# Kernel tuning notes

Measured on AMD Instinct MI355X. Metric: run time of the kernel, lower is better.

The kernel has to match this reference:

```python
import jax, jax.numpy as jnp
import numpy as np

# --- constants derived from init_kwargs (mirrors Categorical2DSemanticMapModule.__init__) ---
H, W = 480, 640
HFOV = 79
DU = 4                      # du_scale
NSEM = 16                   # num_sem_categories
VR = 100                    # vision_range
XY_RES = Z_RES = 5          # map_resolution (cm per bin)
MIN_DEPTH, MAX_DEPTH = 20.0, 500.0   # cm (0.2m/5.0m * 100)
AGENT_H = 88.0              # camera_height * 100 cm
MIN_VOX = int(-40 / Z_RES)  # -8
MAX_VOX = int(360 / Z_RES)  # 72
ZBINS = MAX_VOX - MIN_VOX   # 80
MIN_MAPPED = int(25 / Z_RES - MIN_VOX)             # 13 (min_obs_height_cm)
MAX_MAPPED = int((AGENT_H + 1) / Z_RES - MIN_VOX)  # 25
MAP_T, EXP_T, CAT_T = 1.0, 1.0, 5.0                # map/exp/cat pred thresholds
DILATE_ITER, DILATE_SIZE = 1, 3
F_PIX = (W / 2.0) / float(np.tan(np.deg2rad(HFOV / 2.0)))
CX, CY = W / 2.0, H / 2.0
B, T = 4, 4
LM = 240   # local map size
GM = 960   # global map size
NMAP = 4 + NSEM  # NON_SEM_CHANNELS + num_sem_categories


def setup_inputs() -> dict:
    key = jax.random.key(0)
    k1, k2 = jax.random.split(key)
    seq_obs = jax.random.uniform(k1, (B, T, 4 + NSEM, H, W), dtype=jnp.float32)
    seq_obs = seq_obs.at[:, :, 3].multiply(600.0)  # depth channel in cm, spans [0, 600)
    seq_pose_delta = jax.random.normal(k2, (B, T, 3), dtype=jnp.float32) * 0.1
    seq_camera_poses = jnp.tile(jnp.eye(4, dtype=jnp.float32)[None], (B, 1, 1))
    return {
        'seq_obs': seq_obs,
        'seq_pose_delta': seq_pose_delta,
        'seq_dones': jnp.zeros((B, T), jnp.int32),
        'seq_update_global': jnp.ones((B, T), jnp.int32),
        'seq_camera_poses': seq_camera_poses,
        'init_local_map': jnp.zeros((B, NMAP, LM, LM), jnp.float32),
        'init_global_map': jnp.zeros((B, NMAP, GM, GM), jnp.float32),
        'init_local_pose': jnp.zeros((B, 3), jnp.float32),
        'init_global_pose': jnp.zeros((B, 3), jnp.float32),
        'init_lmb': jnp.zeros((B, 4), jnp.int32),
        'init_origins': jnp.zeros((B, 3), jnp.float32),
    }


def _ego_map(obs_bt):
    """Core semantic-mapping kernel for one frame.
    obs_bt: (4+NSEM, H, W) -> ego map (2+NSEM, VR, VR).
    depth -> point cloud -> voxel scatter-add -> height projection -> threshold -> dilation.
    """
    depth = obs_bt[3, ::DU, ::DU]        # (h, w) cm
    sem = obs_bt[4:, ::DU, ::DU]         # (NSEM, h, w)
    h, w = depth.shape
    uu, vv = jnp.meshgrid(jnp.arange(w, dtype=jnp.float32) * DU,
                          jnp.arange(h, dtype=jnp.float32) * DU)
    # pinhole back-projection (cm), camera at agent height, elevation 0
    X = (uu - CX) * depth / F_PIX            # lateral
    Zh = AGENT_H + (CY - vv) * depth / F_PIX  # height above floor
    Yf = depth                                # forward range
    valid = (depth > MIN_DEPTH) & (depth < MAX_DEPTH)
    # voxel binning (shift_loc centers agent laterally at VR/2)
    xb = jnp.round(X / XY_RES + VR / 2.0).astype(jnp.int32)
    yb = jnp.round(Yf / XY_RES).astype(jnp.int32)
    zb = jnp.round(Zh / Z_RES).astype(jnp.int32) - MIN_VOX
    valid = valid & (xb >= 0) & (xb < VR) & (yb >= 0) & (yb < VR) & (zb >= 0) & (zb < ZBINS)
    lin = (yb * VR + xb) * ZBINS + zb
    lin = jnp.where(valid, lin, VR * VR * ZBINS)  # route invalid points to a dump bin
    C = 1 + NSEM
    feat = jnp.concatenate([jnp.ones((1, h, w), depth.dtype), sem], 0)  # (C, h, w)
    feat = jnp.where(valid[None], feat, 0.0).reshape(C, -1).T           # (N, C)
    grid = jnp.zeros((VR * VR * ZBINS + 1, C), feat.dtype).at[lin.reshape(-1)].add(feat)
    vox = grid[:-1].reshape(VR, VR, ZBINS, C)
    agent_h = vox[:, :, MIN_MAPPED:MAX_MAPPED].sum(2)  # (VR, VR, C)
    all_h = vox.sum(2)
    obstacle = jnp.clip(agent_h[..., 0] / MAP_T, 0.0, 1.0)
    explored = jnp.clip(all_h[..., 0] / EXP_T, 0.0, 1.0)
    semmap = jnp.clip(all_h[..., 1:] / CAT_T, 0.0, 1.0)
    # morphological dilation of obstacle map (3x3 max, dilate_iter times)
    for _ in range(DILATE_ITER):
        obstacle = jax.lax.reduce_window(obstacle, 0.0, jax.lax.max,
                                         (DILATE_SIZE, DILATE_SIZE), (1, 1), 'SAME')
    return jnp.concatenate([obstacle[None], explored[None], jnp.moveaxis(semmap, -1, 0)], 0)


def reference(seq_obs, seq_pose_delta, seq_dones, seq_update_global, seq_camera_poses,
              init_local_map, init_global_map, init_local_pose, init_global_pose,
              init_lmb, init_origins):
    Bb, Tt = seq_obs.shape[:2]
    flat = seq_obs.reshape((Bb * Tt,) + seq_obs.shape[2:])
    ego = jax.vmap(_ego_map)(flat)                      # (B*T, 2+NSEM, VR, VR)
    return ego.reshape(Bb, Tt, 2 + NSEM, VR, VR)
```

## Files before the change

kernel.cpp:

```cpp
#include <hip/hip_runtime.h>
#include <math.h>

#define IMG_H 480
#define IMG_W 640
#define DU    4
#define SUB_H 120
#define SUB_W 160
#define NSEM  16
#define NCH_IN 20
#define VR    100
#define ZBINS 80
#define MIN_MAPPED 13
#define MAX_MAPPED 25
#define NOUT  18
#define NCELL (VR * VR)

__global__ void scatter_kernel(const float* __restrict__ obs,
                               float* __restrict__ out,
                               float* __restrict__ agent,
                               int nframes, float f_pix) {
    const int npix = SUB_H * SUB_W;
    int tid = blockIdx.x * blockDim.x + threadIdx.x;
    if (tid >= nframes * npix) return;
    int f = tid / npix;
    int p = tid - f * npix;
    int v = p / SUB_W;
    int u = p - v * SUB_W;

    const float* frame = obs + (size_t)f * NCH_IN * IMG_H * IMG_W;
    size_t pix_off = (size_t)(v * DU) * IMG_W + (size_t)(u * DU);

    float depth = frame[(size_t)3 * IMG_H * IMG_W + pix_off];
    if (!(depth > 20.0f && depth < 500.0f)) return;

    float uu = (float)(u * DU);
    float vv = (float)(v * DU);
    float X  = (uu - 320.0f) * depth / f_pix;
    float Zh = 88.0f + (240.0f - vv) * depth / f_pix;

    int xb = (int)rintf(X / 5.0f + 50.0f);
    int yb = (int)rintf(depth / 5.0f);
    int zb = (int)rintf(Zh / 5.0f) + 8;

    if (xb < 0 || xb >= VR || yb < 0 || yb >= VR || zb < 0 || zb >= ZBINS) return;

    int cell = yb * VR + xb;
    float* outf = out + (size_t)f * NOUT * NCELL;

    atomicAdd(&outf[1 * NCELL + cell], 1.0f);
    if (zb >= MIN_MAPPED && zb < MAX_MAPPED)
        atomicAdd(&agent[(size_t)f * NCELL + cell], 1.0f);

    #pragma unroll
    for (int c = 0; c < NSEM; ++c) {
        float s = frame[(size_t)(4 + c) * IMG_H * IMG_W + pix_off];
        atomicAdd(&outf[(2 + c) * NCELL + cell], s);
    }
}

__global__ void finalize_kernel(float* __restrict__ out,
                                const float* __restrict__ agent,
                                int nframes) {
    int tid = blockIdx.x * blockDim.x + threadIdx.x;
    if (tid >= nframes * NCELL) return;
    int f = tid / NCELL;
    int p = tid - f * NCELL;
    int y = p / VR;
    int x = p - y * VR;

    const float* ag = agent + (size_t)f * NCELL;
    float m = 0.0f;
    #pragma unroll
    for (int dy = -1; dy <= 1; ++dy) {
        int yy = y + dy;
        if (yy < 0 || yy >= VR) continue;
        #pragma unroll
        for (int dx = -1; dx <= 1; ++dx) {
            int xx = x + dx;
            if (xx < 0 || xx >= VR) continue;
            m = fmaxf(m, ag[yy * VR + xx]);
        }
    }

    float* outf = out + (size_t)f * NOUT * NCELL;
    outf[p] = fminf(m, 1.0f);

    float e = outf[1 * NCELL + p];
    outf[1 * NCELL + p] = fminf(fmaxf(e, 0.0f), 1.0f);

    #pragma unroll
    for (int c = 0; c < NSEM; ++c) {
        float s = outf[(2 + c) * NCELL + p];
        outf[(2 + c) * NCELL + p] = fminf(fmaxf(s / 5.0f, 0.0f), 1.0f);
    }
}

extern "C" void kernel_launch(void* const* d_in, const int* in_sizes, int n_in,
                              void* d_out, int out_size, void* d_ws, size_t ws_size,
                              hipStream_t stream) {
    const float* obs = (const float*)d_in[0];
    float* out = (float*)d_out;
    float* agent = (float*)d_ws;

    int nframes = in_sizes[0] / (NCH_IN * IMG_H * IMG_W);

    float f_pix = (float)(IMG_W / 2.0 / tan((79.0 / 2.0) * M_PI / 180.0));

    hipMemsetAsync(d_out, 0, (size_t)nframes * NOUT * NCELL * sizeof(float), stream);
    hipMemsetAsync(d_ws, 0, (size_t)nframes * NCELL * sizeof(float), stream);

    int npix_total = nframes * SUB_H * SUB_W;
    scatter_kernel<<<(npix_total + 255) / 256, 256, 0, stream>>>(
        obs, out, agent, nframes, f_pix);

    int ncell_total = nframes * NCELL;
    finalize_kernel<<<(ncell_total + 255) / 256, 256, 0, stream>>>(
        out, agent, nframes);
}
```

Before: 711.8 us.

## Fuse scatter and finalize into per-frame-channel kernel with shared-memory histogram

```diff
diff --git a/kernel.cpp b/kernel.cpp
--- a/kernel.cpp
+++ b/kernel.cpp
@@ -6,6 +6,7 @@
 #define DU    4
 #define SUB_H 120
 #define SUB_W 160
+#define NPIX  (SUB_H * SUB_W)
 #define NSEM  16
 #define NCH_IN 20
 #define VR    100
@@ -14,84 +15,80 @@
 #define MAX_MAPPED 25
 #define NOUT  18
 #define NCELL (VR * VR)
+#define NJOBS 18
+#define BLOCK 512
 
-__global__ void scatter_kernel(const float* __restrict__ obs,
-                               float* __restrict__ out,
-                               float* __restrict__ agent,
-                               int nframes, float f_pix) {
-    const int npix = SUB_H * SUB_W;
-    int tid = blockIdx.x * blockDim.x + threadIdx.x;
-    if (tid >= nframes * npix) return;
-    int f = tid / npix;
-    int p = tid - f * npix;
-    int v = p / SUB_W;
-    int u = p - v * SUB_W;
+__global__ __launch_bounds__(BLOCK, 2)
+void ego_map_kernel(const float* __restrict__ obs,
+                    float* __restrict__ out,
+                    float f_pix) {
+    __shared__ float acc[NCELL];
+
+    const int f = blockIdx.x / NJOBS;
+    const int j = blockIdx.x - f * NJOBS;
+    const int tid = threadIdx.x;
+
+    for (int c = tid; c < NCELL; c += BLOCK) acc[c] = 0.0f;
+    __syncthreads();
 
     const float* frame = obs + (size_t)f * NCH_IN * IMG_H * IMG_W;
-    size_t pix_off = (size_t)(v * DU) * IMG_W + (size_t)(u * DU);
+    const float* depth_ch = frame + (size_t)3 * IMG_H * IMG_W;
+    const float* sem_ch   = (j >= 2) ? frame + (size_t)(4 + (j - 2)) * IMG_H * IMG_W
+                                     : depth_ch;
 
-    float depth = frame[(size_t)3 * IMG_H * IMG_W + pix_off];
-    if (!(depth > 20.0f && depth < 500.0f)) return;
+    for (int p = tid; p < NPIX; p += BLOCK) {
+        int v = p / SUB_W;
+        int u = p - v * SUB_W;
+        size_t pix_off = (size_t)(v * DU) * IMG_W + (size_t)(u * DU);
 
-    float uu = (float)(u * DU);
-    float vv = (float)(v * DU);
-    float X  = (uu - 320.0f) * depth / f_pix;
-    float Zh = 88.0f + (240.0f - vv) * depth / f_pix;
+        float depth = depth_ch[pix_off];
+        if (!(depth > 20.0f && depth < 500.0f)) continue;
 
-    int xb = (int)rintf(X / 5.0f + 50.0f);
-    int yb = (int)rintf(depth / 5.0f);
-    int zb = (int)rintf(Zh / 5.0f) + 8;
+        float uu = (float)(u * DU);
+        float vv = (float)(v * DU);
+        float X  = (uu - 320.0f) * depth / f_pix;
+        float Zh = 88.0f + (240.0f - vv) * depth / f_pix;
 
-    if (xb < 0 || xb >= VR || yb < 0 || yb >= VR || zb < 0 || zb >= ZBINS) return;
+        int xb = (int)rintf(X / 5.0f + 50.0f);
+        int yb = (int)rintf(depth / 5.0f);
+        int zb = (int)rintf(Zh / 5.0f) + 8;
 
-    int cell = yb * VR + xb;
+        if (xb < 0 || xb >= VR || yb < 0 || yb >= VR || zb < 0 || zb >= ZBINS)
+            continue;
+
+        int cell = yb * VR + xb;
+        if (j == 0) {
+            if (zb >= MIN_MAPPED && zb < MAX_MAPPED)
+                atomicAdd(&acc[cell], 1.0f);
+        } else if (j == 1) {
+            atomicAdd(&acc[cell], 1.0f);
+        } else {
+            atomicAdd(&acc[cell], sem_ch[pix_off]);
+        }
+    }
+    __syncthreads();
+
     float* outf = out + (size_t)f * NOUT * NCELL;
 
-    atomicAdd(&outf[1 * NCELL + cell], 1.0f);
-    if (zb >= MIN_MAPPED && zb < MAX_MAPPED)
-        atomicAdd(&agent[(size_t)f * NCELL + cell], 1.0f);
-
-    #pragma unroll
-    for (int c = 0; c < NSEM; ++c) {
-        float s = frame[(size_t)(4 + c) * IMG_H * IMG_W + pix_off];
-        atomicAdd(&outf[(2 + c) * NCELL + cell], s);
-    }
-}
-
-__global__ void finalize_kernel(float* __restrict__ out,
-                                const float* __restrict__ agent,
-                                int nframes) {
-    int tid = blockIdx.x * blockDim.x + threadIdx.x;
-    if (tid >= nframes * NCELL) return;
-    int f = tid / NCELL;
-    int p = tid - f * NCELL;
-    int y = p / VR;
-    int x = p - y * VR;
-
-    const float* ag = agent + (size_t)f * NCELL;
-    float m = 0.0f;
-    #pragma unroll
-    for (int dy = -1; dy <= 1; ++dy) {
-        int yy = y + dy;
-        if (yy < 0 || yy >= VR) continue;
-        #pragma unroll
-        for (int dx = -1; dx <= 1; ++dx) {
-            int xx = x + dx;
-            if (xx < 0 || xx >= VR) continue;
-            m = fmaxf(m, ag[yy * VR + xx]);
+    if (j == 0) {
+        for (int c = tid; c < NCELL; c += BLOCK) {
+            int y = c / VR;
+            int x = c - y * VR;
+            float m = 0.0f;
+            int y0 = (y > 0) ? y - 1 : 0, y1 = (y < VR - 1) ? y + 1 : VR - 1;
+            int x0 = (x > 0) ? x - 1 : 0, x1 = (x < VR - 1) ? x + 1 : VR - 1;
+            for (int yy = y0; yy <= y1; ++yy)
+                for (int xx = x0; xx <= x1; ++xx)
+                    m = fmaxf(m, acc[yy * VR + xx]);
+            outf[c] = fminf(m, 1.0f);
         }
-    }
-
-    float* outf = out + (size_t)f * NOUT * NCELL;
-    outf[p] = fminf(m, 1.0f);
-
-    float e = outf[1 * NCELL + p];
-    outf[1 * NCELL + p] = fminf(fmaxf(e, 0.0f), 1.0f);
-
-    #pragma unroll
-    for (int c = 0; c < NSEM; ++c) {
-        float s = outf[(2 + c) * NCELL + p];
-        outf[(2 + c) * NCELL + p] = fminf(fmaxf(s / 5.0f, 0.0f), 1.0f);
+    } else if (j == 1) {
+        for (int c = tid; c < NCELL; c += BLOCK)
+            outf[NCELL + c] = fminf(fmaxf(acc[c], 0.0f), 1.0f);
+    } else {
+        float* oc = outf + (size_t)j * NCELL;
+        for (int c = tid; c < NCELL; c += BLOCK)
+            oc[c] = fminf(fmaxf(acc[c] / 5.0f, 0.0f), 1.0f);
     }
 }
 
@@ -100,20 +97,10 @@
                               hipStream_t stream) {
     const float* obs = (const float*)d_in[0];
     float* out = (float*)d_out;
-    float* agent = (float*)d_ws;
 
     int nframes = in_sizes[0] / (NCH_IN * IMG_H * IMG_W);
 
     float f_pix = (float)(IMG_W / 2.0 / tan((79.0 / 2.0) * M_PI / 180.0));
 
-    hipMemsetAsync(d_out, 0, (size_t)nframes * NOUT * NCELL * sizeof(float), stream);
-    hipMemsetAsync(d_ws, 0, (size_t)nframes * NCELL * sizeof(float), stream);
-
-    int npix_total = nframes * SUB_H * SUB_W;
-    scatter_kernel<<<(npix_total + 255) / 256, 256, 0, stream>>>(
-        obs, out, agent, nframes, f_pix);
-
-    int ncell_total = nframes * NCELL;
-    finalize_kernel<<<(ncell_total + 255) / 256, 256, 0, stream>>>(
-        out, agent, nframes);
+    ego_map_kernel<<<nframes * NJOBS, BLOCK, 0, stream>>>(obs, out, f_pix);
 }
```

Result: faster. 605.2 us (-15.0%).
